# Optimization experiments

Measured on AMD Instinct MI355X. Metric: run time of the kernel, lower is better.

## Reference

```python
import math
import jax, jax.numpy as jnp
import numpy as np

D = 512
H = 8
N_COLS = 2048            # n + 1
D_COL = math.ceil(2 * math.log2(N_COLS))  # 22
B = 8
N_KEEP = 768
T = N_KEEP + 1


def setup_inputs() -> dict:
    key = jax.random.key(0)
    ks = jax.random.split(key, 12)
    inp = {
        "x_head": jax.random.normal(ks[0], (B, T, D), jnp.float32),
        "x_tail": jax.random.normal(ks[1], (B, T, D), jnp.float32),
        "ids_keep": jax.random.randint(ks[2], (B, N_KEEP), 0, N_COLS - 1),
        # W_tail is tied to W_head (sym_weight=True)
        "W_head_w": jax.random.normal(ks[3], (D, D), jnp.float32) * (1.0 / math.sqrt(D)),
        "W_head_b": jnp.zeros((D,), jnp.float32),
        "W_v_w": jax.random.normal(ks[4], (D, D), jnp.float32) * (1.0 / math.sqrt(D)),
        "W_v_b": jnp.zeros((D,), jnp.float32),
        "W_out_w": jax.random.normal(ks[5], (D, D), jnp.float32) * (1.0 / math.sqrt(D)),
        "W_out_b": jnp.zeros((D,), jnp.float32),
        "rel_emb": jnp.ones((H, D // H), jnp.float32),
        "col_head": jax.random.normal(ks[6], (H, N_COLS, D_COL), jnp.float32),
        "col_tail": jax.random.normal(ks[7], (H, N_COLS, D_COL), jnp.float32),
        "bias": jnp.zeros((1,), jnp.float32),
    }
    return inp


def _split_heads(x, n_heads):
    b, t, d = x.shape
    return x.reshape(b, t, n_heads, d // n_heads).transpose(0, 2, 1, 3)  # [B,H,T,dh]


def _gather_cols(col_emb, ids_keep):
    """col_emb: [H, N_COLS, d_col] (L2-normalized). Gather kept feature rows per
    batch element and re-prepend the CLS/readout row -> [B, H, 1+n_keep, d_col]."""
    cls = col_emb[:, :1, :]                       # [H,1,dc]
    feats = col_emb[:, 1:, :]                     # [H,N_COLS-1,dc]
    kept = jnp.take(feats, ids_keep, axis=1)      # [H,B,nk,dc]
    kept = kept.transpose(1, 0, 2, 3)             # [B,H,nk,dc]
    cls_b = jnp.broadcast_to(cls[None], (kept.shape[0],) + cls.shape)  # [B,H,1,dc]
    return jnp.concatenate([cls_b, kept], axis=2)


def reference(x_head, x_tail, ids_keep, W_head_w, W_head_b, W_v_w, W_v_b,
              W_out_w, W_out_b, rel_emb, col_head, col_tail, bias):
    n_heads = rel_emb.shape[0]
    d_head = rel_emb.shape[1]
    b, t, _ = x_head.shape

    # Projections (W_tail tied to W_head)
    f_head = x_head @ W_head_w.T + W_head_b
    f_tail = x_tail @ W_head_w.T + W_head_b
    f_v = x_tail @ W_v_w.T + W_v_b

    fh = _split_heads(f_head, n_heads)  # [B,H,T,dh]
    ft = _split_heads(f_tail, n_heads)
    fv = _split_heads(f_v, n_heads)

    # relation-weighted score: f_head @ diag(rel_emb) @ f_tail^T / sqrt(dh)
    weight_score = jnp.einsum('bhqd,bhkd->bhqk', fh * rel_emb[None, :, None, :], ft)
    weight_score = weight_score / math.sqrt(d_head)

    # Normalized topology embeddings + masked-token gather
    ch = col_head / jnp.linalg.norm(col_head, axis=-1, keepdims=True)
    ct = col_tail / jnp.linalg.norm(col_tail, axis=-1, keepdims=True)
    ch = _gather_cols(ch, ids_keep)  # [B,H,T,dc]
    ct = _gather_cols(ct, ids_keep)
    top_score = jnp.einsum('bhqd,bhkd->bhqk', ch, ct)  # [B,H,T,T]

    # Topology -> straight-through binary adjacency
    adj_probs = jax.nn.sigmoid(top_score + bias[0])
    nsi_mask = 1.0 - jnp.eye(t, dtype=adj_probs.dtype)          # no self-interaction
    adj_probs = adj_probs * nsi_mask
    readout_mask = jnp.ones((t,), adj_probs.dtype).at[0].set(0.0)  # prune edges to readout
    adj_probs = adj_probs * readout_mask
    adj = (adj_probs > 0.5).astype(adj_probs.dtype) - jax.lax.stop_gradient(adj_probs) + adj_probs

    adj_mask = (1.0 - adj) * -10000.0
    fr_graph = jax.nn.softmax(weight_score + adj_mask, axis=-1)

    x = jnp.einsum('bhqk,bhkd->bhqd', fr_graph, fv)
    x = x.transpose(0, 2, 1, 3).reshape(b, t, n_heads * fv.shape[-1])
    x = x @ W_out_w.T + W_out_b
    return (x, jax.lax.stop_gradient(fr_graph))
```

## Files before the change

### kernel.cpp

```cpp
#include <hip/hip_runtime.h>

#define D_     512
#define H_     8
#define NCOLS_ 2048
#define DCOL_  22
#define B_     8
#define NKEEP_ 768
#define T_     769
#define BT_    (B_*T_)
#define BH_    (B_*H_)

typedef __attribute__((ext_vector_type(8))) short bf16x8;
typedef __attribute__((ext_vector_type(4))) float f32x4;

__device__ __forceinline__ ushort f2bf(float f) {
    unsigned u = __float_as_uint(f);
    unsigned r = u + 0x7fffu + ((u >> 16) & 1u);
    return (ushort)(r >> 16);
}
__device__ __forceinline__ float bf2f(ushort u) {
    return __uint_as_float(((unsigned)u) << 16);
}

__global__ __launch_bounds__(256) void proj_mfma(
    const float* __restrict__ xh, const float* __restrict__ xt,
    const ushort* __restrict__ x1b,
    const float* __restrict__ Wh, const float* __restrict__ Wv,
    const float* __restrict__ Wo,
    const float* __restrict__ bh_, const float* __restrict__ bv_,
    const float* __restrict__ bo_, const float* __restrict__ rel,
    ushort* __restrict__ fhb, ushort* __restrict__ ftb,
    ushort* __restrict__ fvb, float* __restrict__ xout, const int jobParam)
{
    __shared__ __align__(16) ushort As[128*40];
    __shared__ __align__(16) ushort Bs[128*40];
    const int job = (jobParam < 0) ? (int)blockIdx.z : jobParam;
    const float* A32 = nullptr; const ushort* A16 = nullptr;
    const float* W; const float* bias;
    ushort* outb = nullptr; float* outf = nullptr; int mode;
    if (job == 0)      { A32 = xh; W = Wh; bias = bh_; outb = fhb; mode = 0; }
    else if (job == 1) { A32 = xt; W = Wh; bias = bh_; outb = ftb; mode = 1; }
    else if (job == 2) { A32 = xt; W = Wv; bias = bv_; outb = fvb; mode = 1; }
    else               { A16 = x1b; W = Wo; bias = bo_; outf = xout; mode = 3; }

    const int t    = threadIdx.x;
    const int lane = t & 63;
    const int wv   = t >> 6;
    const int wr   = wv >> 1, wc = wv & 1;
    const int m16  = lane & 15, q4 = lane >> 4;
    const int m0   = blockIdx.y * 128;
    const int n0   = blockIdx.x * 128;

    f32x4 acc[4][4] = {};
    for (int k0 = 0; k0 < 512; k0 += 32) {
        {
            const int sr = t >> 1, sh = t & 1;
            const int row = m0 + sr;
            ushort ta[16];
            if (A16) {
                bf16x8 z = {}; bf16x8 v0 = z, v1 = z;
                if (row < BT_) {
                    const bf16x8* gp = (const bf16x8*)(A16 + (size_t)row*512 + k0 + sh*16);
                    v0 = gp[0]; v1 = gp[1];
                }
                *(bf16x8*)&ta[0] = v0; *(bf16x8*)&ta[8] = v1;
            } else {
                #pragma unroll
                for (int e = 0; e < 16; ++e) ta[e] = 0;
                if (row < BT_) {
                    const float* ap = A32 + (size_t)row*512 + k0 + sh*16;
                    #pragma unroll
                    for (int e = 0; e < 4; ++e) {
                        float4 f = *(const float4*)(ap + e*4);
                        ta[e*4+0]=f2bf(f.x); ta[e*4+1]=f2bf(f.y);
                        ta[e*4+2]=f2bf(f.z); ta[e*4+3]=f2bf(f.w);
                    }
                }
            }
            *(bf16x8*)&As[sr*40 + sh*16]     = *(bf16x8*)&ta[0];
            *(bf16x8*)&As[sr*40 + sh*16 + 8] = *(bf16x8*)&ta[8];
            const float* wp = W + (size_t)(n0 + sr)*512 + k0 + sh*16;
            ushort tw[16];
            #pragma unroll
            for (int e = 0; e < 4; ++e) {
                float4 f = *(const float4*)(wp + e*4);
                tw[e*4+0]=f2bf(f.x); tw[e*4+1]=f2bf(f.y);
                tw[e*4+2]=f2bf(f.z); tw[e*4+3]=f2bf(f.w);
            }
            *(bf16x8*)&Bs[sr*40 + sh*16]     = *(bf16x8*)&tw[0];
            *(bf16x8*)&Bs[sr*40 + sh*16 + 8] = *(bf16x8*)&tw[8];
        }
        __syncthreads();
        bf16x8 a[4], b[4];
        #pragma unroll
        for (int i = 0; i < 4; ++i)
            a[i] = *(const bf16x8*)&As[(wr*64 + i*16 + m16)*40 + q4*8];
        #pragma unroll
        for (int j = 0; j < 4; ++j)
            b[j] = *(const bf16x8*)&Bs[(wc*64 + j*16 + m16)*40 + q4*8];
        #pragma unroll
        for (int i = 0; i < 4; ++i)
            #pragma unroll
            for (int j = 0; j < 4; ++j)
                acc[i][j] = __builtin_amdgcn_mfma_f32_16x16x32_bf16(a[i], b[j], acc[i][j], 0, 0, 0);
        __syncthreads();
    }

    #pragma unroll
    for (int j = 0; j < 4; ++j) {
        const int n = n0 + wc*64 + j*16 + m16;
        const float bn = bias[n];
        const float sc = (mode == 0) ? rel[n] * 0.125f : 1.0f;
        const int h = n >> 6, dh = n & 63;
        #pragma unroll
        for (int i = 0; i < 4; ++i) {
            #pragma unroll
            for (int r = 0; r < 4; ++r) {
                int m = m0 + wr*64 + i*16 + q4*4 + r;
                if (m >= BT_) continue;
                float v = acc[i][j][r] + bn;
                if (mode == 3) {
                    outf[(size_t)m*512 + n] = v;
                } else {
                    if (mode == 0) v *= sc;
                    int bb = m / T_, tt = m - bb*T_;
                    outb[(((size_t)bb*H_ + h)*T_ + tt)*64 + dh] = f2bf(v);
                }
            }
        }
    }
}

__global__ void gather_norm(
    const float* __restrict__ col_head, const float* __restrict__ col_tail,
    const int* __restrict__ ids, float* __restrict__ chg, float* __restrict__ ctg)
{
    int r = blockIdx.x * blockDim.x + threadIdx.x;
    const int total = BH_ * T_;
    if (r >= 2*total) return;
    const bool tail = (r >= total);
    int rr = tail ? r - total : r;
    int bh = rr / T_;
    int q  = rr - bh*T_;
    int b  = bh >> 3, h = bh & 7;
    int src = (q == 0) ? 0 : (1 + ids[b*NKEEP_ + q - 1]);
    const float* cp = (tail ? col_tail : col_head) + ((size_t)h*NCOLS_ + src)*DCOL_;
    float v[DCOL_];
    float ss = 0.f;
    #pragma unroll
    for (int j = 0; j < DCOL_; ++j) { v[j] = cp[j]; ss += v[j]*v[j]; }
    float inv = 1.0f / sqrtf(ss);
    float* op = (tail ? ctg : chg) + (size_t)rr*DCOL_;
    #pragma unroll
    for (int j = 0; j < DCOL_; ++j) op[j] = v[j]*inv;
}

__global__ __launch_bounds__(256) void fused_attn(
    const ushort* __restrict__ fhb, const ushort* __restrict__ ftb,
    const ushort* __restrict__ fvb, const float* __restrict__ chg,
    const float* __restrict__ ctg, const float* __restrict__ biasp,
    float* __restrict__ fr, ushort* __restrict__ x1b, float* __restrict__ invA)
{
    __shared__ __align__(16) ushort Qs[64*72];
    __shared__ __align__(16) ushort Ks[64*72];
    __shared__ __align__(16) ushort Vs[64*72];
    __shared__ __align__(16) ushort Et[64*72];
    __shared__ __align__(16) float  Gq[DCOL_*68];
    __shared__ __align__(16) float  Gk[DCOL_*68];
    __shared__ float sumP[4*64];
    __shared__ float inv_s[64];

    const int bh = blockIdx.y;
    const int q0 = blockIdx.x * 64;
    const int t    = threadIdx.x;
    const int lane = t & 63, w = t >> 6;
    const int m16  = lane & 15, q4 = lane >> 4;
    const float bias0 = biasp[0];

    {
        int qr = t >> 2, qc = min(q0 + qr, T_-1);
        const ushort* qp = fhb + ((size_t)bh*T_ + qc)*64 + (t&3)*16;
        *(bf16x8*)&Qs[qr*72 + (t&3)*16]     = *(const bf16x8*)qp;
        *(bf16x8*)&Qs[qr*72 + (t&3)*16 + 8] = *(const bf16x8*)(qp + 8);
    }
    for (int idx = t; idx < 64*DCOL_; idx += 256) {
        int r = idx / DCOL_, d = idx - r*DCOL_;
        int qc = min(q0 + r, T_-1);
        Gq[d*68 + r] = chg[((size_t)bh*T_ + qc)*DCOL_ + d];
    }

    float psum[4][4] = {};
    f32x4 Oacc[4] = {};

    for (int kt = 0; kt < 13; ++kt) {
        const int k0g = kt*64;
        __syncthreads();
        {
            int kr = t >> 2, kc = min(k0g + kr, T_-1);
            const ushort* kp = ftb + ((size_t)bh*T_ + kc)*64 + (t&3)*16;
            *(bf16x8*)&Ks[kr*72 + (t&3)*16]     = *(const bf16x8*)kp;
            *(bf16x8*)&Ks[kr*72 + (t&3)*16 + 8] = *(const bf16x8*)(kp + 8);
            const ushort* vp = fvb + ((size_t)bh*T_ + kc)*64 + (t&3)*16;
            bf16x8 v0 = *(const bf16x8*)vp, v1 = *(const bf16x8*)(vp + 8);
            int dbase = (t&3)*16;
            #pragma unroll
            for (int e = 0; e < 8; ++e) Vs[(dbase+e)*72 + kr]   = (ushort)v0[e];
            #pragma unroll
            for (int e = 0; e < 8; ++e) Vs[(dbase+8+e)*72 + kr] = (ushort)v1[e];
        }
        for (int idx = t; idx < 64*DCOL_; idx += 256) {
            int r = idx / DCOL_, d = idx - r*DCOL_;
            int kc = min(k0g + r, T_-1);
            Gk[d*68 + r] = ctg[((size_t)bh*T_ + kc)*DCOL_ + d];
        }
        __syncthreads();

        const int kL = w*16 + m16;
        const int kg = k0g + kL;
        unsigned kmask = 0;
        {
            float ga[4][4] = {};
            #pragma unroll 2
            for (int d = 0; d < DCOL_; ++d) {
                float gk = Gk[d*68 + kL];
                #pragma unroll
                for (int i = 0; i < 4; ++i) {
                    float4 a4 = *(const float4*)&Gq[d*68 + i*16 + q4*4];
                    ga[i][0] += a4.x*gk; ga[i][1] += a4.y*gk;
                    ga[i][2] += a4.z*gk; ga[i][3] += a4.w*gk;
                }
            }
            const bool kok = (kg != 0) && (kg < T_);
            #pragma unroll
            for (int i = 0; i < 4; ++i)
                #pragma unroll
                for (int r = 0; r < 4; ++r) {
                    int qg = q0 + i*16 + q4*4 + r;
                    if (kok && (ga[i][r] + bias0 > 0.f) && (qg != kg))
                        kmask |= 1u << (i*4 + r);
                }
        }

        f32x4 Sacc[4] = {};
        #pragma unroll
        for (int step = 0; step < 2; ++step) {
            bf16x8 b = *(const bf16x8*)&Ks[kL*72 + step*32 + q4*8];
            #pragma unroll
            for (int i = 0; i < 4; ++i) {
                bf16x8 a = *(const bf16x8*)&Qs[(i*16 + m16)*72 + step*32 + q4*8];
                Sacc[i] = __builtin_amdgcn_mfma_f32_16x16x32_bf16(a, b, Sacc[i], 0, 0, 0);
            }
        }

        #pragma unroll
        for (int i = 0; i < 4; ++i) {
            #pragma unroll
            for (int r = 0; r < 4; ++r) {
                float e = ((kmask >> (i*4 + r)) & 1u) ? __expf(Sacc[i][r]) : 0.f;
                psum[i][r] += e;
                Et[(i*16 + q4*4 + r)*72 + kL] = f2bf(e);
            }
        }
        __syncthreads();

        #pragma unroll
        for (int step = 0; step < 2; ++step) {
            bf16x8 a = *(const bf16x8*)&Et[(w*16 + m16)*72 + step*32 + q4*8];
            #pragma unroll
            for (int j = 0; j < 4; ++j) {
                bf16x8 b = *(const bf16x8*)&Vs[(j*16 + m16)*72 + step*32 + q4*8];
                Oacc[j] = __builtin_amdgcn_mfma_f32_16x16x32_bf16(a, b, Oacc[j], 0, 0, 0);
            }
        }

        {
            const int c = t & 15;
            #pragma unroll
            for (int p = 0; p < 4; ++p) {
                int row = p*16 + (t >> 4);
                int qg = q0 + row;
                if (qg >= T_) continue;
                char* rowbase = (char*)(fr + ((size_t)bh*T_ + qg)*T_);
                #pragma unroll
                for (int e = 0; e < 2; ++e) {
                    int dw = c + 16*e;
                    int kk = k0g + dw*2;
                    unsigned u = *(const unsigned*)&Et[row*72 + dw*2];
                    if (kk + 1 < T_)      *(unsigned*)(rowbase + (size_t)kk*2) = u;
                    else if (kk < T_)     *(ushort*)(rowbase + (size_t)kk*2) = (ushort)u;
                }
            }
        }
    }

    #pragma unroll
    for (int i = 0; i < 4; ++i)
        #pragma unroll
        for (int r = 0; r < 4; ++r) {
            float v = psum[i][r];
            v += __shfl_xor(v, 1, 64);
            v += __shfl_xor(v, 2, 64);
            v += __shfl_xor(v, 4, 64);
            v += __shfl_xor(v, 8, 64);
            psum[i][r] = v;
        }
    if (m16 == 0) {
        #pragma unroll
        for (int i = 0; i < 4; ++i)
            #pragma unroll
            for (int r = 0; r < 4; ++r)
                sumP[w*64 + i*16 + q4*4 + r] = psum[i][r];
    }
    __syncthreads();
    if (t < 64) {
        float s = sumP[t] + sumP[64+t] + sumP[128+t] + sumP[192+t];
        float iv = 1.0f / fmaxf(s, 1e-30f);
        inv_s[t] = iv;
        if (q0 + t < T_) invA[(size_t)bh*T_ + q0 + t] = iv;
    }
    __syncthreads();

    {
        const int b = bh >> 3, h = bh & 7;
        #pragma unroll
        for (int j = 0; j < 4; ++j) {
            int d = j*16 + m16;
            #pragma unroll
            for (int r = 0; r < 4; ++r) {
                int rr = w*16 + q4*4 + r;
                int qg = q0 + rr;
                if (qg < T_)
                    x1b[((size_t)b*T_ + qg)*512 + h*64 + d] = f2bf(Oacc[j][r] * inv_s[rr]);
            }
        }
    }
}

__global__ __launch_bounds__(256) void normalize_fr(
    float* __restrict__ fr, const float* __restrict__ invA)
{
    const int row = blockIdx.x;
    const int t = threadIdx.x;
    float* rowp = fr + (size_t)row * T_;
    const ushort* packed = (const ushort*)rowp;
    const float iv = invA[row];
    float v0 = bf2f(packed[t])       * iv;
    float v1 = bf2f(packed[t + 256]) * iv;
    float v2 = bf2f(packed[t + 512]) * iv;
    float v3 = 0.f;
    if (t == 0) v3 = bf2f(packed[768]) * iv;
    __syncthreads();
    rowp[t]       = v0;
    rowp[t + 256] = v1;
    rowp[t + 512] = v2;
    if (t == 0) rowp[768] = v3;
}

extern "C" void kernel_launch(void* const* d_in, const int* in_sizes, int n_in,
                              void* d_out, int out_size, void* d_ws, size_t ws_size,
                              hipStream_t stream)
{
    (void)in_sizes; (void)n_in; (void)out_size; (void)ws_size;
    const float* x_head   = (const float*)d_in[0];
    const float* x_tail   = (const float*)d_in[1];
    const int*   ids      = (const int*)  d_in[2];
    const float* W_head_w = (const float*)d_in[3];
    const float* W_head_b = (const float*)d_in[4];
    const float* W_v_w    = (const float*)d_in[5];
    const float* W_v_b    = (const float*)d_in[6];
    const float* W_out_w  = (const float*)d_in[7];
    const float* W_out_b  = (const float*)d_in[8];
    const float* rel      = (const float*)d_in[9];
    const float* col_h    = (const float*)d_in[10];
    const float* col_t    = (const float*)d_in[11];
    const float* biasp    = (const float*)d_in[12];

    const size_t F   = (size_t)BH_*T_*64;
    const size_t C22 = (size_t)BH_*T_*DCOL_;

    char* ws = (char*)d_ws;
    ushort* fhb = (ushort*)ws;   ws += F*2;
    ushort* ftb = (ushort*)ws;   ws += F*2;
    ushort* fvb = (ushort*)ws;   ws += F*2;
    ushort* x1b = (ushort*)ws;   ws += F*2;
    float*  chg = (float*)ws;    ws += C22*4;
    float*  ctg = (float*)ws;    ws += C22*4;
    float*  invA = (float*)ws;   ws += (size_t)BH_*T_*4;

    float* xout = (float*)d_out;
    float* fr   = xout + (size_t)BT_*D_;

    dim3 blk(256, 1, 1);

    gather_norm<<<(2*BH_*T_ + 255)/256, blk, 0, stream>>>(col_h, col_t, ids, chg, ctg);

    proj_mfma<<<dim3(4, 49, 3), blk, 0, stream>>>(
        x_head, x_tail, nullptr, W_head_w, W_v_w, W_out_w,
        W_head_b, W_v_b, W_out_b, rel, fhb, ftb, fvb, nullptr, -1);

    fused_attn<<<dim3(13, BH_), blk, 0, stream>>>(
        fhb, ftb, fvb, chg, ctg, biasp, fr, x1b, invA);

    normalize_fr<<<BH_*T_, blk, 0, stream>>>(fr, invA);

    proj_mfma<<<dim3(4, 49, 1), blk, 0, stream>>>(
        x_head, x_tail, x1b, W_head_w, W_v_w, W_out_w,
        W_head_b, W_v_b, W_out_b, rel, fhb, ftb, fvb, xout, 3);
}
```

Measured before the change: 454.1 us.

## Compute topology scores with split-fp16 MFMA, prefetch K/V tiles, swizzle V LDS

The fp32 scalar 22-dim topology dot product in the attention kernel is replaced by MFMA f16 products on hi/lo split fp16 embeddings, which gather_norm now also emits padded to 32. Scores within a small margin of the threshold fall back to an exact fp32 dot from global memory. The change also register-prefetches the next K/V/topology tile before the barrier, XOR-swizzles the transposed V layout in LDS to reduce bank conflicts, remaps block indices, and sets occupancy launch bounds. The goal is to cut ALU and LDS cost in the mask computation, at the price of extra workspace writes and occasional divergent exact-check paths.

```diff
diff --git a/kernel.cpp b/kernel.cpp
--- a/kernel.cpp
+++ b/kernel.cpp
@@ -11,6 +11,7 @@
 #define BH_    (B_*H_)
 
 typedef __attribute__((ext_vector_type(8))) short bf16x8;
+typedef __attribute__((ext_vector_type(8))) _Float16 f16x8;
 typedef __attribute__((ext_vector_type(4))) float f32x4;
 
 __device__ __forceinline__ ushort f2bf(float f) {
@@ -20,6 +21,15 @@
 }
 __device__ __forceinline__ float bf2f(ushort u) {
     return __uint_as_float(((unsigned)u) << 16);
+}
+
+__device__ __attribute__((noinline)) float exact_dot22(
+    const float* __restrict__ qp, const float* __restrict__ kp)
+{
+    float s = 0.f;
+    #pragma unroll
+    for (int d2 = 0; d2 < DCOL_; ++d2) s += qp[d2]*kp[d2];
+    return s;
 }
 
 __global__ __launch_bounds__(256) void proj_mfma(
@@ -133,7 +143,9 @@
 
 __global__ void gather_norm(
     const float* __restrict__ col_head, const float* __restrict__ col_tail,
-    const int* __restrict__ ids, float* __restrict__ chg, float* __restrict__ ctg)
+    const int* __restrict__ ids, float* __restrict__ chg, float* __restrict__ ctg,
+    ushort* __restrict__ chH, ushort* __restrict__ chL,
+    ushort* __restrict__ ctH, ushort* __restrict__ ctL)
 {
     int r = blockIdx.x * blockDim.x + threadIdx.x;
     const int total = BH_ * T_;
@@ -151,31 +163,63 @@
     for (int j = 0; j < DCOL_; ++j) { v[j] = cp[j]; ss += v[j]*v[j]; }
     float inv = 1.0f / sqrtf(ss);
     float* op = (tail ? ctg : chg) + (size_t)rr*DCOL_;
-    #pragma unroll
-    for (int j = 0; j < DCOL_; ++j) op[j] = v[j]*inv;
-}
-
-__global__ __launch_bounds__(256) void fused_attn(
+    ushort* hp = (tail ? ctH : chH) + (size_t)rr*32;
+    ushort* lp = (tail ? ctL : chL) + (size_t)rr*32;
+    #pragma unroll
+    for (int j = 0; j < DCOL_; ++j) {
+        float x = v[j]*inv;
+        op[j] = x;
+        float xs = x * 32.f;
+        _Float16 hh = (_Float16)xs;
+        float res = (xs - (float)hh) * 2048.f;
+        _Float16 ll = (_Float16)res;
+        hp[j] = __builtin_bit_cast(ushort, hh);
+        lp[j] = __builtin_bit_cast(ushort, ll);
+    }
+    #pragma unroll
+    for (int j = DCOL_; j < 32; ++j) { hp[j] = 0; lp[j] = 0; }
+}
+
+__global__ __launch_bounds__(256, 3) void fused_attn(
     const ushort* __restrict__ fhb, const ushort* __restrict__ ftb,
     const ushort* __restrict__ fvb, const float* __restrict__ chg,
-    const float* __restrict__ ctg, const float* __restrict__ biasp,
+    const float* __restrict__ ctg,
+    const ushort* __restrict__ chH, const ushort* __restrict__ chL,
+    const ushort* __restrict__ ctH, const ushort* __restrict__ ctL,
+    const float* __restrict__ biasp,
     float* __restrict__ fr, ushort* __restrict__ x1b, float* __restrict__ invA)
 {
     __shared__ __align__(16) ushort Qs[64*72];
     __shared__ __align__(16) ushort Ks[64*72];
     __shared__ __align__(16) ushort Vs[64*72];
     __shared__ __align__(16) ushort Et[64*72];
-    __shared__ __align__(16) float  Gq[DCOL_*68];
-    __shared__ __align__(16) float  Gk[DCOL_*68];
+    __shared__ __align__(16) ushort KH[64*40];
+    __shared__ __align__(16) ushort KL[64*40];
     __shared__ float sumP[4*64];
     __shared__ float inv_s[64];
 
-    const int bh = blockIdx.y;
-    const int q0 = blockIdx.x * 64;
+    const int flat = (int)blockIdx.y * 13 + (int)blockIdx.x;
+    const int swz  = (flat & 7) * 104 + (flat >> 3);
+    const int bh   = swz / 13;
+    const int q0   = (swz - bh*13) * 64;
+
     const int t    = threadIdx.x;
     const int lane = t & 63, w = t >> 6;
     const int m16  = lane & 15, q4 = lane >> 4;
     const float bias0 = biasp[0];
+
+    const int pkr = t >> 2, pqt = t & 3;
+    bf16x8 pK0, pK1, pV0, pV1, pH, pL;
+    auto issue_tile = [&](int kt) {
+        int kc = min(kt*64 + pkr, T_-1);
+        const ushort* kp = ftb + ((size_t)bh*T_ + kc)*64 + pqt*16;
+        pK0 = *(const bf16x8*)kp; pK1 = *(const bf16x8*)(kp + 8);
+        const ushort* vp = fvb + ((size_t)bh*T_ + kc)*64 + pqt*16;
+        pV0 = *(const bf16x8*)vp; pV1 = *(const bf16x8*)(vp + 8);
+        pH = *(const bf16x8*)(ctH + ((size_t)bh*T_ + kc)*32 + pqt*8);
+        pL = *(const bf16x8*)(ctL + ((size_t)bh*T_ + kc)*32 + pqt*8);
+    };
+    issue_tile(0);
 
     {
         int qr = t >> 2, qc = min(q0 + qr, T_-1);
@@ -183,10 +227,12 @@
         *(bf16x8*)&Qs[qr*72 + (t&3)*16]     = *(const bf16x8*)qp;
         *(bf16x8*)&Qs[qr*72 + (t&3)*16 + 8] = *(const bf16x8*)(qp + 8);
     }
-    for (int idx = t; idx < 64*DCOL_; idx += 256) {
-        int r = idx / DCOL_, d = idx - r*DCOL_;
-        int qc = min(q0 + r, T_-1);
-        Gq[d*68 + r] = chg[((size_t)bh*T_ + qc)*DCOL_ + d];
+    f16x8 gqh[4], gql[4];
+    #pragma unroll
+    for (int i = 0; i < 4; ++i) {
+        int qc = min(q0 + i*16 + m16, T_-1);
+        gqh[i] = *(const f16x8*)(chH + ((size_t)bh*T_ + qc)*32 + q4*8);
+        gql[i] = *(const f16x8*)(chL + ((size_t)bh*T_ + qc)*32 + q4*8);
     }
 
     float psum[4][4] = {};
@@ -195,56 +241,67 @@
     for (int kt = 0; kt < 13; ++kt) {
         const int k0g = kt*64;
         __syncthreads();
+
+        *(bf16x8*)&Ks[pkr*72 + pqt*16]     = pK0;
+        *(bf16x8*)&Ks[pkr*72 + pqt*16 + 8] = pK1;
         {
-            int kr = t >> 2, kc = min(k0g + kr, T_-1);
-            const ushort* kp = ftb + ((size_t)bh*T_ + kc)*64 + (t&3)*16;
-            *(bf16x8*)&Ks[kr*72 + (t&3)*16]     = *(const bf16x8*)kp;
-            *(bf16x8*)&Ks[kr*72 + (t&3)*16 + 8] = *(const bf16x8*)(kp + 8);
-            const ushort* vp = fvb + ((size_t)bh*T_ + kc)*64 + (t&3)*16;
-            bf16x8 v0 = *(const bf16x8*)vp, v1 = *(const bf16x8*)(vp + 8);
-            int dbase = (t&3)*16;
-            #pragma unroll
-            for (int e = 0; e < 8; ++e) Vs[(dbase+e)*72 + kr]   = (ushort)v0[e];
-            #pragma unroll
-            for (int e = 0; e < 8; ++e) Vs[(dbase+8+e)*72 + kr] = (ushort)v1[e];
-        }
-        for (int idx = t; idx < 64*DCOL_; idx += 256) {
-            int r = idx / DCOL_, d = idx - r*DCOL_;
-            int kc = min(k0g + r, T_-1);
-            Gk[d*68 + r] = ctg[((size_t)bh*T_ + kc)*DCOL_ + d];
-        }
+            const int dbase = pqt*16;
+            #pragma unroll
+            for (int e = 0; e < 8; ++e) {
+                int d = dbase + e;
+                Vs[d*72 + (((pkr>>3) ^ (d>>3))<<3) + (pkr&7)] = (ushort)pV0[e];
+            }
+            #pragma unroll
+            for (int e = 0; e < 8; ++e) {
+                int d = dbase + 8 + e;
+                Vs[d*72 + (((pkr>>3) ^ (d>>3))<<3) + (pkr&7)] = (ushort)pV1[e];
+            }
+        }
+        *(bf16x8*)&KH[pkr*40 + pqt*8] = pH;
+        *(bf16x8*)&KL[pkr*40 + pqt*8] = pL;
+
+        if (kt + 1 < 13) issue_tile(kt + 1);
         __syncthreads();
 
-        const int kL = w*16 + m16;
-        const int kg = k0g + kL;
+        const int kL2 = w*16 + m16;
+        const int kg  = k0g + kL2;
         unsigned kmask = 0;
         {
-            float ga[4][4] = {};
-            #pragma unroll 2
-            for (int d = 0; d < DCOL_; ++d) {
-                float gk = Gk[d*68 + kL];
+            f16x8 bhf = *(const f16x8*)&KH[kL2*40 + q4*8];
+            f16x8 blf = *(const f16x8*)&KL[kL2*40 + q4*8];
+            f32x4 G1[4] = {}; f32x4 G2[4] = {};
+            #pragma unroll
+            for (int i = 0; i < 4; ++i) {
+                G1[i] = __builtin_amdgcn_mfma_f32_16x16x32_f16(gqh[i], bhf, G1[i], 0, 0, 0);
+                G2[i] = __builtin_amdgcn_mfma_f32_16x16x32_f16(gqh[i], blf, G2[i], 0, 0, 0);
+                G2[i] = __builtin_amdgcn_mfma_f32_16x16x32_f16(gql[i], bhf, G2[i], 0, 0, 0);
+            }
+            const bool kok = (kg != 0) && (kg < T_);
+            if (kok) {
+                const float bS = bias0 * 1024.f;
                 #pragma unroll
                 for (int i = 0; i < 4; ++i) {
-                    float4 a4 = *(const float4*)&Gq[d*68 + i*16 + q4*4];
-                    ga[i][0] += a4.x*gk; ga[i][1] += a4.y*gk;
-                    ga[i][2] += a4.z*gk; ga[i][3] += a4.w*gk;
+                    #pragma unroll
+                    for (int r = 0; r < 4; ++r) {
+                        int qg = q0 + i*16 + q4*4 + r;
+                        if (qg == kg) continue;
+                        float sd = G1[i][r] + G2[i][r]*(1.0f/2048.0f) + bS;
+                        bool keep = sd > 0.f;
+                        if (__builtin_fabsf(sd) <= 0.16f && qg < T_) {
+                            float s = exact_dot22(chg + ((size_t)bh*T_ + qg)*DCOL_,
+                                                  ctg + ((size_t)bh*T_ + kg)*DCOL_);
+                            keep = (s + bias0 > 0.f);
+                        }
+                        if (keep) kmask |= 1u << (i*4 + r);
+                    }
                 }
             }
-            const bool kok = (kg != 0) && (kg < T_);
-            #pragma unroll
-            for (int i = 0; i < 4; ++i)
-                #pragma unroll
-                for (int r = 0; r < 4; ++r) {
-                    int qg = q0 + i*16 + q4*4 + r;
-                    if (kok && (ga[i][r] + bias0 > 0.f) && (qg != kg))
-                        kmask |= 1u << (i*4 + r);
-                }
         }
 
         f32x4 Sacc[4] = {};
         #pragma unroll
         for (int step = 0; step < 2; ++step) {
-            bf16x8 b = *(const bf16x8*)&Ks[kL*72 + step*32 + q4*8];
+            bf16x8 b = *(const bf16x8*)&Ks[kL2*72 + step*32 + q4*8];
             #pragma unroll
             for (int i = 0; i < 4; ++i) {
                 bf16x8 a = *(const bf16x8*)&Qs[(i*16 + m16)*72 + step*32 + q4*8];
@@ -258,7 +315,7 @@
             for (int r = 0; r < 4; ++r) {
                 float e = ((kmask >> (i*4 + r)) & 1u) ? __expf(Sacc[i][r]) : 0.f;
                 psum[i][r] += e;
-                Et[(i*16 + q4*4 + r)*72 + kL] = f2bf(e);
+                Et[(i*16 + q4*4 + r)*72 + kL2] = f2bf(e);
             }
         }
         __syncthreads();
@@ -268,7 +325,8 @@
             bf16x8 a = *(const bf16x8*)&Et[(w*16 + m16)*72 + step*32 + q4*8];
             #pragma unroll
             for (int j = 0; j < 4; ++j) {
-                bf16x8 b = *(const bf16x8*)&Vs[(j*16 + m16)*72 + step*32 + q4*8];
+                int dv = j*16 + m16;
+                bf16x8 b = *(const bf16x8*)&Vs[dv*72 + (((step*4 + q4) ^ (dv>>3))<<3)];
                 Oacc[j] = __builtin_amdgcn_mfma_f32_16x16x32_bf16(a, b, Oacc[j], 0, 0, 0);
             }
         }
@@ -377,6 +435,7 @@
 
     const size_t F   = (size_t)BH_*T_*64;
     const size_t C22 = (size_t)BH_*T_*DCOL_;
+    const size_t C32 = (size_t)BH_*T_*32;
 
     char* ws = (char*)d_ws;
     ushort* fhb = (ushort*)ws;   ws += F*2;
@@ -386,20 +445,25 @@
     float*  chg = (float*)ws;    ws += C22*4;
     float*  ctg = (float*)ws;    ws += C22*4;
     float*  invA = (float*)ws;   ws += (size_t)BH_*T_*4;
+    ushort* chH = (ushort*)ws;   ws += C32*2;
+    ushort* chL = (ushort*)ws;   ws += C32*2;
+    ushort* ctH = (ushort*)ws;   ws += C32*2;
+    ushort* ctL = (ushort*)ws;   ws += C32*2;
 
     float* xout = (float*)d_out;
     float* fr   = xout + (size_t)BT_*D_;
 
     dim3 blk(256, 1, 1);
 
-    gather_norm<<<(2*BH_*T_ + 255)/256, blk, 0, stream>>>(col_h, col_t, ids, chg, ctg);
+    gather_norm<<<(2*BH_*T_ + 255)/256, blk, 0, stream>>>(
+        col_h, col_t, ids, chg, ctg, chH, chL, ctH, ctL);
 
     proj_mfma<<<dim3(4, 49, 3), blk, 0, stream>>>(
         x_head, x_tail, nullptr, W_head_w, W_v_w, W_out_w,
         W_head_b, W_v_b, W_out_b, rel, fhb, ftb, fvb, nullptr, -1);
 
     fused_attn<<<dim3(13, BH_), blk, 0, stream>>>(
-        fhb, ftb, fvb, chg, ctg, biasp, fr, x1b, invA);
+        fhb, ftb, fvb, chg, ctg, chH, chL, ctH, ctL, biasp, fr, x1b, invA);
 
     normalize_fr<<<BH_*T_, blk, 0, stream>>>(fr, invA);
 
```

Result: slower. 578.4 us (+27.4%).
